# Optimization experiments

Measured on AMD Instinct MI355X. Metric: run time of the kernel, lower is better.

The kernel has to match this reference:

```python
import jax, jax.numpy as jnp
import numpy as np

B, MENU, N, M = 4096, 256, 8, 16


def setup_inputs() -> dict:
    key = jax.random.key(0)
    k1, k2, k3, k4 = jax.random.split(key, 4)
    input_bids = jax.random.uniform(k1, (B, N, M), dtype=jnp.float32)
    allocs = jax.random.uniform(k2, (B, MENU, N, M), dtype=jnp.float32)
    # bidder weights must be strictly positive (divided by in payments)
    w = jax.random.uniform(k3, (B, N), dtype=jnp.float32, minval=0.5, maxval=1.5)
    b = jax.random.normal(k4, (B, MENU), dtype=jnp.float32)
    softmax_temp = jnp.asarray(100.0, dtype=jnp.float32)
    return {"input_bids": input_bids, "allocs": allocs, "w": w, "b": b,
            "softmax_temp": softmax_temp}


def reference(input_bids, allocs, w, b, softmax_temp):
    Bsz, n, m = input_bids.shape
    # append the "null" menu entry (zero allocation, zero boost)
    allocs = jnp.concatenate([allocs, jnp.zeros((Bsz, 1, n, m), allocs.dtype)], axis=1)  # B,S,n,m
    b = jnp.concatenate([b, jnp.zeros((Bsz, 1), b.dtype)], axis=1)                        # B,S

    # utility of each agent under each menu entry
    util = jnp.einsum('bsnm,bnm->bsn', allocs, input_bids)        # B,S,n
    per_agent_welfare = w[:, None, :] * util                      # B,S,n
    total_welfare = per_agent_welfare.sum(-1)                     # B,S

    alloc_choice = jax.nn.softmax((total_welfare + b) * softmax_temp, axis=-1)  # B,S
    item_allocation = jnp.einsum('bs,bsnm->bnm', alloc_choice, allocs)          # B,n,m
    chosen_welfare = jnp.einsum('bsn,bs->bn', per_agent_welfare, alloc_choice)  # B,n

    # leave-one-out (VCG-style) payments, vectorized over the removed agent i
    mask = 1.0 - jnp.eye(n, dtype=per_agent_welfare.dtype)        # n,n; row i zeros agent i
    removed_welfare = per_agent_welfare[None] * mask[:, None, None, :]  # i,B,S,n
    total_removed = removed_welfare.sum(-1)                       # i,B,S
    removed_choice = jax.nn.softmax((total_removed + b[None]) * softmax_temp, axis=-1)  # i,B,S

    removed_chosen_sum = jnp.einsum('ibsn,ibs->ib', removed_welfare, removed_choice)  # i,B
    masked_chosen_sum = jnp.einsum('bn,in->ib', chosen_welfare, mask)                 # i,B
    removed_b = jnp.einsum('ibs,bs->ib', removed_choice, b)                           # i,B
    alloc_b = jnp.einsum('bs,bs->b', alloc_choice, b)                                 # B

    payments = (removed_chosen_sum + removed_b - masked_chosen_sum - alloc_b[None]) / w.T  # n,B
    return alloc_choice, item_allocation, payments, allocs
```

## Files before the change

kernel.cpp:

```cpp
#include <hip/hip_runtime.h>

#define NAGENTS 8
#define NM 128
#define MENU 256
#define SFULL 257

#define BAR() asm volatile("s_waitcnt lgkmcnt(0)\n\ts_barrier" ::: "memory")

__device__ __forceinline__ float wredmax(float v) {
#pragma unroll
    for (int o = 32; o; o >>= 1) v = fmaxf(v, __shfl_xor(v, o));
    return v;
}
__device__ __forceinline__ float wredsum(float v) {
#pragma unroll
    for (int o = 32; o; o >>= 1) v += __shfl_xor(v, o);
    return v;
}

__global__ __launch_bounds__(1024, 4) void cama_kernel(
    const float* __restrict__ bids,
    const float* __restrict__ allocs,
    const float* __restrict__ wvec,
    const float* __restrict__ bvec,
    const float* __restrict__ tempp,
    float* __restrict__ out, int Bsz, int iters)
{
    __shared__ float lds_pwT[NAGENTS * MENU];
    __shared__ float lds_tot[MENU];
    __shared__ float lds_bb[2][MENU];
    __shared__ __align__(16) float lds_bids[2][NM];
    __shared__ float lds_w[2][NAGENTS];
    __shared__ float lds_ch[SFULL];
    __shared__ __align__(16) float lds_scr[16 * NM];
    __shared__ float lds_rcs[NAGENTS], lds_rb[NAGENTS], lds_cw[NAGENTS];
    __shared__ float lds_ab;

    const int u = threadIdx.x;
    const int lane = u & 63;
    const int wave = u >> 6;
    const int n  = (u >> 2) & 7;
    const int mq = u & 3;
    const int su = u >> 5;

    float* out_choice = out;
    float* out_item   = out + (size_t)Bsz * SFULL;
    float* out_pay    = out_item + (size_t)Bsz * NM;
    float* out_all    = out_pay + (size_t)NAGENTS * Bsz;
    float4* out_all4  = (float4*)out_all;
    const float4* all4 = (const float4*)allocs;

    const float temp = tempp[0];
    size_t a = (size_t)blockIdx.x * iters;

    float4 Pf[8];

    {
        float rbb = 0.f, rbid = 0.f, rw = 0.f;
        if (u < MENU)    rbb  = bvec[a * MENU + u];
        if (u < NM)      rbid = bids[a * NM + u];
        if (u < NAGENTS) rw   = wvec[a * NAGENTS + u];
#pragma unroll
        for (int k = 0; k < 8; ++k)
            Pf[k] = all4[a * 8192 + (k << 10) + u];
        if (u < MENU)    lds_bb[0][u]   = rbb;
        if (u < NM)      lds_bids[0][u] = rbid;
        if (u < NAGENTS) lds_w[0][u]    = rw;
    }
    BAR();

    for (int it = 0; it < iters; ++it) {
        const int p = it & 1;
        const size_t an = (it + 1 < iters) ? a + 1 : a;

        const float4 q4 = ((const float4*)&lds_bids[p][0])[u & 31];
        const float w_n = lds_w[p][n];

        float4 Sf[8];
#pragma unroll
        for (int k = 0; k < 8; ++k) {
            Sf[k] = Pf[k];
            Pf[k] = all4[an * 8192 + (k << 10) + u];
            out_all4[a * 8224 + (k << 10) + u] = Sf[k];
            const int s = (k << 5) + su;
            float util = Sf[k].x*q4.x + Sf[k].y*q4.y + Sf[k].z*q4.z + Sf[k].w*q4.w;
            util += __shfl_xor(util, 1);
            util += __shfl_xor(util, 2);
            float pwv = w_n * util;
            if (mq == 0) lds_pwT[(n << 8) + (s ^ (n << 2))] = pwv;
            float t = pwv;
            t += __shfl_xor(t, 4);
            t += __shfl_xor(t, 8);
            t += __shfl_xor(t, 16);
            if ((lane & 31) == 0) lds_tot[s] = t;
        }
        if (u < 32)
            out_all4[a * 8224 + 8192 + u] = make_float4(0.f, 0.f, 0.f, 0.f);

        float rbb2 = 0.f, rbid2 = 0.f, rw2 = 0.f;
        if (u < MENU)    rbb2  = bvec[an * MENU + u];
        if (u < NM)      rbid2 = bids[an * NM + u];
        if (u < NAGENTS) rw2   = wvec[an * NAGENTS + u];
        BAR();

        if (wave == 0) {
            float xs[4], bl[4], es[4];
            float mx = -1e30f;
#pragma unroll
            for (int c = 0; c < 4; ++c) {
                int v = (c << 6) | lane;
                bl[c] = lds_bb[p][v];
                float x = (lds_tot[v] + bl[c]) * temp;
                xs[c] = x; mx = fmaxf(mx, x);
            }
            mx = fmaxf(wredmax(mx), 0.f);
            float se = 0.f, sab = 0.f;
#pragma unroll
            for (int c = 0; c < 4; ++c) { es[c] = __expf(xs[c] - mx); se += es[c]; sab += es[c] * bl[c]; }
            float en = __expf(-mx);
            se = wredsum(se) + en;
            sab = wredsum(sab);
            float inv = 1.f / se;
#pragma unroll
            for (int c = 0; c < 4; ++c) {
                int v = (c << 6) | lane;
                float chv = es[c] * inv;
                lds_ch[v] = chv;
                out_choice[a * SFULL + v] = chv;
            }
            if (lane == 0) {
                float chn = en * inv;
                lds_ch[MENU] = chn;
                out_choice[a * SFULL + MENU] = chn;
                lds_ab = sab * inv;
            }
        } else if (wave <= 8) {
            const int i = wave - 1;
            float xs[4], trs[4], bl[4];
            float mx = -1e30f;
#pragma unroll
            for (int c = 0; c < 4; ++c) {
                int v = (c << 6) | lane;
                bl[c] = lds_bb[p][v];
                float tr = lds_tot[v] - lds_pwT[(i << 8) + (v ^ (i << 2))];
                trs[c] = tr;
                float x = (tr + bl[c]) * temp;
                xs[c] = x; mx = fmaxf(mx, x);
            }
            mx = fmaxf(wredmax(mx), 0.f);
            float se = 0.f, s1 = 0.f, s2 = 0.f;
#pragma unroll
            for (int c = 0; c < 4; ++c) {
                float e = __expf(xs[c] - mx);
                se += e; s1 += e * trs[c]; s2 += e * bl[c];
            }
            se = wredsum(se) + __expf(-mx);
            s1 = wredsum(s1);
            s2 = wredsum(s2);
            if (lane == 0) { lds_rcs[i] = s1 / se; lds_rb[i] = s2 / se; }
        }
        BAR();

        if (wave < 8) {
            const int i = wave;
            float cwv = 0.f;
#pragma unroll
            for (int c = 0; c < 4; ++c) {
                int v = (c << 6) | lane;
                cwv += lds_ch[v] * lds_pwT[(i << 8) + (v ^ (i << 2))];
            }
            cwv = wredsum(cwv);
            if (lane == 0) lds_cw[i] = cwv;
        }
        {
            float ax = 0.f, ay = 0.f, az = 0.f, aw = 0.f;
#pragma unroll
            for (int k = 0; k < 8; ++k) {
                float chv = lds_ch[(k << 5) + su];
                ax += Sf[k].x * chv; ay += Sf[k].y * chv;
                az += Sf[k].z * chv; aw += Sf[k].w * chv;
            }
            ax += __shfl_xor(ax, 32);
            ay += __shfl_xor(ay, 32);
            az += __shfl_xor(az, 32);
            aw += __shfl_xor(aw, 32);
            if (lane < 32)
                ((float4*)lds_scr)[(wave << 5) + lane] = make_float4(ax, ay, az, aw);
        }
        if (u < MENU)    lds_bb[p ^ 1][u]   = rbb2;
        if (u < NM)      lds_bids[p ^ 1][u] = rbid2;
        if (u < NAGENTS) lds_w[p ^ 1][u]    = rw2;
        BAR();

        if (u < NM) {
            float s = 0.f;
#pragma unroll
            for (int w = 0; w < 16; ++w) s += lds_scr[(w << 7) + u];
            out_item[a * NM + u] = s;
        }
        if (u < NAGENTS) {
            float ctot = 0.f;
#pragma unroll
            for (int k = 0; k < NAGENTS; ++k) ctot += lds_cw[k];
            float pay = (lds_rcs[u] + lds_rb[u] - (ctot - lds_cw[u]) - lds_ab)
                        / lds_w[p][u];
            out_pay[(size_t)u * Bsz + a] = pay;
        }
        a = a + 1;
    }
}

extern "C" void kernel_launch(void* const* d_in, const int* in_sizes, int n_in,
                              void* d_out, int out_size, void* d_ws, size_t ws_size,
                              hipStream_t stream) {
    const float* bids   = (const float*)d_in[0];
    const float* allocs = (const float*)d_in[1];
    const float* wvec   = (const float*)d_in[2];
    const float* bvec   = (const float*)d_in[3];
    const float* tempp  = (const float*)d_in[4];
    float* out = (float*)d_out;
    const int Bsz = in_sizes[0] / NM;
    const int nblocks = 256;
    const int iters = Bsz / nblocks;
    cama_kernel<<<nblocks, 1024, 0, stream>>>(bids, allocs, wvec, bvec, tempp,
                                              out, Bsz, iters);
}
```

Measured before the change: 259.6 us.

## Use one 256-thread block per batch row with online-softmax item allocation

Replaces the persistent 256-block, 1024-thread kernel that software-pipelined allocs loads across iterations with one 256-thread block per batch element. The item allocation is now accumulated during the streaming pass with an online (running max / rescaled) softmax, then merged across halves and waves. This removes the register-held allocs tile and one barrier phase. In exchange it drops the explicit cross-iteration prefetch and relies on many resident blocks to hide memory latency, and it adds extra exp work per element.

New measurement: 235.3 us. -9.4%, faster.

```diff
diff --git a/kernel.cpp b/kernel.cpp
--- a/kernel.cpp
+++ b/kernel.cpp
@@ -18,195 +18,202 @@
     return v;
 }
 
-__global__ __launch_bounds__(1024, 4) void cama_kernel(
+__global__ __launch_bounds__(256, 8) void cama_kernel(
     const float* __restrict__ bids,
     const float* __restrict__ allocs,
     const float* __restrict__ wvec,
     const float* __restrict__ bvec,
     const float* __restrict__ tempp,
-    float* __restrict__ out, int Bsz, int iters)
+    float* __restrict__ out, int Bsz)
 {
     __shared__ float lds_pwT[NAGENTS * MENU];
     __shared__ float lds_tot[MENU];
-    __shared__ float lds_bb[2][MENU];
-    __shared__ __align__(16) float lds_bids[2][NM];
-    __shared__ float lds_w[2][NAGENTS];
+    __shared__ float lds_bb[MENU];
     __shared__ float lds_ch[SFULL];
-    __shared__ __align__(16) float lds_scr[16 * NM];
+    __shared__ __align__(16) float4 lds_accs[4][32];
+    __shared__ __align__(8)  float2 lds_mz[4][32];
     __shared__ float lds_rcs[NAGENTS], lds_rb[NAGENTS], lds_cw[NAGENTS];
     __shared__ float lds_ab;
 
     const int u = threadIdx.x;
     const int lane = u & 63;
     const int wave = u >> 6;
-    const int n  = (u >> 2) & 7;
-    const int mq = u & 3;
+    const int c = u & 31;
+    const int n = c >> 2;
     const int su = u >> 5;
+    const size_t bb_ = (size_t)blockIdx.x;
 
     float* out_choice = out;
     float* out_item   = out + (size_t)Bsz * SFULL;
     float* out_pay    = out_item + (size_t)Bsz * NM;
     float* out_all    = out_pay + (size_t)NAGENTS * Bsz;
-    float4* out_all4  = (float4*)out_all;
-    const float4* all4 = (const float4*)allocs;
+    float4* out_all4  = (float4*)out_all + bb_ * 8224;
+    const float4* src4 = (const float4*)allocs + bb_ * 8192;
 
     const float temp = tempp[0];
-    size_t a = (size_t)blockIdx.x * iters;
-
-    float4 Pf[8];
+    lds_bb[u] = bvec[bb_ * MENU + u];
+    const float4 q4 = ((const float4*)(bids + bb_ * NM))[c];
+    const float w_n = wvec[bb_ * NAGENTS + n];
+    BAR();
+
+    float m_r = -1e30f, Z_r = 0.f;
+    float4 acc = make_float4(0.f, 0.f, 0.f, 0.f);
+#pragma unroll 4
+    for (int k = 0; k < 32; ++k) {
+        const int idx = (k << 8) + u;
+        float4 a4 = src4[idx];
+        out_all4[idx] = a4;
+        const int s = (k << 3) + su;
+        float util = a4.x*q4.x + a4.y*q4.y + a4.z*q4.z + a4.w*q4.w;
+        util += __shfl_xor(util, 1);
+        util += __shfl_xor(util, 2);
+        float pwv = w_n * util;
+        if ((u & 3) == 0) lds_pwT[(n << 8) + (s ^ (n << 2))] = pwv;
+        float t = pwv;
+        t += __shfl_xor(t, 4);
+        t += __shfl_xor(t, 8);
+        t += __shfl_xor(t, 16);
+        if (c == 0) lds_tot[s] = t;
+        float x = (t + lds_bb[s]) * temp;
+        float mn = fmaxf(m_r, x);
+        float sc = __expf(m_r - mn);
+        float p  = __expf(x - mn);
+        Z_r = Z_r * sc + p;
+        acc.x = acc.x * sc + p * a4.x;
+        acc.y = acc.y * sc + p * a4.y;
+        acc.z = acc.z * sc + p * a4.z;
+        acc.w = acc.w * sc + p * a4.w;
+        m_r = mn;
+    }
+    if (u < 32)
+        out_all4[8192 + u] = make_float4(0.f, 0.f, 0.f, 0.f);
 
     {
-        float rbb = 0.f, rbid = 0.f, rw = 0.f;
-        if (u < MENU)    rbb  = bvec[a * MENU + u];
-        if (u < NM)      rbid = bids[a * NM + u];
-        if (u < NAGENTS) rw   = wvec[a * NAGENTS + u];
-#pragma unroll
-        for (int k = 0; k < 8; ++k)
-            Pf[k] = all4[a * 8192 + (k << 10) + u];
-        if (u < MENU)    lds_bb[0][u]   = rbb;
-        if (u < NM)      lds_bids[0][u] = rbid;
-        if (u < NAGENTS) lds_w[0][u]    = rw;
-    }
-    BAR();
-
-    for (int it = 0; it < iters; ++it) {
-        const int p = it & 1;
-        const size_t an = (it + 1 < iters) ? a + 1 : a;
-
-        const float4 q4 = ((const float4*)&lds_bids[p][0])[u & 31];
-        const float w_n = lds_w[p][n];
-
-        float4 Sf[8];
-#pragma unroll
-        for (int k = 0; k < 8; ++k) {
-            Sf[k] = Pf[k];
-            Pf[k] = all4[an * 8192 + (k << 10) + u];
-            out_all4[a * 8224 + (k << 10) + u] = Sf[k];
-            const int s = (k << 5) + su;
-            float util = Sf[k].x*q4.x + Sf[k].y*q4.y + Sf[k].z*q4.z + Sf[k].w*q4.w;
-            util += __shfl_xor(util, 1);
-            util += __shfl_xor(util, 2);
-            float pwv = w_n * util;
-            if (mq == 0) lds_pwT[(n << 8) + (s ^ (n << 2))] = pwv;
-            float t = pwv;
-            t += __shfl_xor(t, 4);
-            t += __shfl_xor(t, 8);
-            t += __shfl_xor(t, 16);
-            if ((lane & 31) == 0) lds_tot[s] = t;
-        }
-        if (u < 32)
-            out_all4[a * 8224 + 8192 + u] = make_float4(0.f, 0.f, 0.f, 0.f);
-
-        float rbb2 = 0.f, rbid2 = 0.f, rw2 = 0.f;
-        if (u < MENU)    rbb2  = bvec[an * MENU + u];
-        if (u < NM)      rbid2 = bids[an * NM + u];
-        if (u < NAGENTS) rw2   = wvec[an * NAGENTS + u];
-        BAR();
-
-        if (wave == 0) {
+        float mo = __shfl_xor(m_r, 32);
+        float Zo = __shfl_xor(Z_r, 32);
+        float ax = __shfl_xor(acc.x, 32), ay = __shfl_xor(acc.y, 32);
+        float az = __shfl_xor(acc.z, 32), aw = __shfl_xor(acc.w, 32);
+        float mn = fmaxf(m_r, mo);
+        float s0 = __expf(m_r - mn), s1 = __expf(mo - mn);
+        Z_r = Z_r * s0 + Zo * s1;
+        acc.x = acc.x * s0 + ax * s1;
+        acc.y = acc.y * s0 + ay * s1;
+        acc.z = acc.z * s0 + az * s1;
+        acc.w = acc.w * s0 + aw * s1;
+        if (lane < 32) {
+            lds_accs[wave][c] = acc;
+            lds_mz[wave][c] = make_float2(mn, Z_r);
+        }
+    }
+    BAR();
+
+    for (int t = wave; t < 9; t += 4) {
+        if (t == 0) {
             float xs[4], bl[4], es[4];
             float mx = -1e30f;
 #pragma unroll
-            for (int c = 0; c < 4; ++c) {
-                int v = (c << 6) | lane;
-                bl[c] = lds_bb[p][v];
-                float x = (lds_tot[v] + bl[c]) * temp;
-                xs[c] = x; mx = fmaxf(mx, x);
+            for (int c4 = 0; c4 < 4; ++c4) {
+                int v = (c4 << 6) | lane;
+                bl[c4] = lds_bb[v];
+                float x = (lds_tot[v] + bl[c4]) * temp;
+                xs[c4] = x; mx = fmaxf(mx, x);
             }
             mx = fmaxf(wredmax(mx), 0.f);
             float se = 0.f, sab = 0.f;
 #pragma unroll
-            for (int c = 0; c < 4; ++c) { es[c] = __expf(xs[c] - mx); se += es[c]; sab += es[c] * bl[c]; }
+            for (int c4 = 0; c4 < 4; ++c4) {
+                es[c4] = __expf(xs[c4] - mx);
+                se += es[c4]; sab += es[c4] * bl[c4];
+            }
             float en = __expf(-mx);
             se = wredsum(se) + en;
             sab = wredsum(sab);
             float inv = 1.f / se;
 #pragma unroll
-            for (int c = 0; c < 4; ++c) {
-                int v = (c << 6) | lane;
-                float chv = es[c] * inv;
+            for (int c4 = 0; c4 < 4; ++c4) {
+                int v = (c4 << 6) | lane;
+                float chv = es[c4] * inv;
                 lds_ch[v] = chv;
-                out_choice[a * SFULL + v] = chv;
+                out_choice[bb_ * SFULL + v] = chv;
             }
             if (lane == 0) {
                 float chn = en * inv;
                 lds_ch[MENU] = chn;
-                out_choice[a * SFULL + MENU] = chn;
+                out_choice[bb_ * SFULL + MENU] = chn;
                 lds_ab = sab * inv;
             }
-        } else if (wave <= 8) {
-            const int i = wave - 1;
+        } else {
+            const int i = t - 1;
             float xs[4], trs[4], bl[4];
             float mx = -1e30f;
 #pragma unroll
-            for (int c = 0; c < 4; ++c) {
-                int v = (c << 6) | lane;
-                bl[c] = lds_bb[p][v];
+            for (int c4 = 0; c4 < 4; ++c4) {
+                int v = (c4 << 6) | lane;
+                bl[c4] = lds_bb[v];
                 float tr = lds_tot[v] - lds_pwT[(i << 8) + (v ^ (i << 2))];
-                trs[c] = tr;
-                float x = (tr + bl[c]) * temp;
-                xs[c] = x; mx = fmaxf(mx, x);
+                trs[c4] = tr;
+                float x = (tr + bl[c4]) * temp;
+                xs[c4] = x; mx = fmaxf(mx, x);
             }
             mx = fmaxf(wredmax(mx), 0.f);
             float se = 0.f, s1 = 0.f, s2 = 0.f;
 #pragma unroll
-            for (int c = 0; c < 4; ++c) {
-                float e = __expf(xs[c] - mx);
-                se += e; s1 += e * trs[c]; s2 += e * bl[c];
+            for (int c4 = 0; c4 < 4; ++c4) {
+                float e = __expf(xs[c4] - mx);
+                se += e; s1 += e * trs[c4]; s2 += e * bl[c4];
             }
             se = wredsum(se) + __expf(-mx);
             s1 = wredsum(s1);
             s2 = wredsum(s2);
             if (lane == 0) { lds_rcs[i] = s1 / se; lds_rb[i] = s2 / se; }
         }
-        BAR();
-
-        if (wave < 8) {
-            const int i = wave;
-            float cwv = 0.f;
-#pragma unroll
-            for (int c = 0; c < 4; ++c) {
-                int v = (c << 6) | lane;
-                cwv += lds_ch[v] * lds_pwT[(i << 8) + (v ^ (i << 2))];
-            }
-            cwv = wredsum(cwv);
-            if (lane == 0) lds_cw[i] = cwv;
-        }
-        {
-            float ax = 0.f, ay = 0.f, az = 0.f, aw = 0.f;
-#pragma unroll
-            for (int k = 0; k < 8; ++k) {
-                float chv = lds_ch[(k << 5) + su];
-                ax += Sf[k].x * chv; ay += Sf[k].y * chv;
-                az += Sf[k].z * chv; aw += Sf[k].w * chv;
-            }
-            ax += __shfl_xor(ax, 32);
-            ay += __shfl_xor(ay, 32);
-            az += __shfl_xor(az, 32);
-            aw += __shfl_xor(aw, 32);
-            if (lane < 32)
-                ((float4*)lds_scr)[(wave << 5) + lane] = make_float4(ax, ay, az, aw);
-        }
-        if (u < MENU)    lds_bb[p ^ 1][u]   = rbb2;
-        if (u < NM)      lds_bids[p ^ 1][u] = rbid2;
-        if (u < NAGENTS) lds_w[p ^ 1][u]    = rw2;
-        BAR();
-
-        if (u < NM) {
-            float s = 0.f;
-#pragma unroll
-            for (int w = 0; w < 16; ++w) s += lds_scr[(w << 7) + u];
-            out_item[a * NM + u] = s;
-        }
-        if (u < NAGENTS) {
-            float ctot = 0.f;
-#pragma unroll
-            for (int k = 0; k < NAGENTS; ++k) ctot += lds_cw[k];
-            float pay = (lds_rcs[u] + lds_rb[u] - (ctot - lds_cw[u]) - lds_ab)
-                        / lds_w[p][u];
-            out_pay[(size_t)u * Bsz + a] = pay;
-        }
-        a = a + 1;
+    }
+    BAR();
+
+    for (int i = wave; i < NAGENTS; i += 4) {
+        float cwv = 0.f;
+#pragma unroll
+        for (int c4 = 0; c4 < 4; ++c4) {
+            int v = (c4 << 6) | lane;
+            cwv += lds_ch[v] * lds_pwT[(i << 8) + (v ^ (i << 2))];
+        }
+        cwv = wredsum(cwv);
+        if (lane == 0) lds_cw[i] = cwv;
+    }
+    if (u < 32) {
+        float4 A = lds_accs[0][u];
+        float2 mz = lds_mz[0][u];
+        float M = mz.x, Z = mz.y;
+#pragma unroll
+        for (int j = 1; j < 4; ++j) {
+            float4 Aj = lds_accs[j][u];
+            float2 mzj = lds_mz[j][u];
+            float mn = fmaxf(M, mzj.x);
+            float s0 = __expf(M - mn), s1 = __expf(mzj.x - mn);
+            Z = Z * s0 + mzj.y * s1;
+            A.x = A.x * s0 + Aj.x * s1;
+            A.y = A.y * s0 + Aj.y * s1;
+            A.z = A.z * s0 + Aj.z * s1;
+            A.w = A.w * s0 + Aj.w * s1;
+            M = mn;
+        }
+        float mn = fmaxf(M, 0.f);
+        float s0 = __expf(M - mn);
+        Z = Z * s0 + __expf(-mn);
+        float inv = 1.f / Z;
+        s0 *= inv;
+        ((float4*)(out_item + bb_ * NM))[u] =
+            make_float4(A.x * s0, A.y * s0, A.z * s0, A.w * s0);
+    }
+    BAR();
+
+    if (u < NAGENTS) {
+        float ctot = 0.f;
+#pragma unroll
+        for (int k = 0; k < NAGENTS; ++k) ctot += lds_cw[k];
+        float pay = (lds_rcs[u] + lds_rb[u] - (ctot - lds_cw[u]) - lds_ab)
+                    / wvec[bb_ * NAGENTS + u];
+        out_pay[(size_t)u * Bsz + bb_] = pay;
     }
 }
 
@@ -220,8 +227,6 @@
     const float* tempp  = (const float*)d_in[4];
     float* out = (float*)d_out;
     const int Bsz = in_sizes[0] / NM;
-    const int nblocks = 256;
-    const int iters = Bsz / nblocks;
-    cama_kernel<<<nblocks, 1024, 0, stream>>>(bids, allocs, wvec, bvec, tempp,
-                                              out, Bsz, iters);
-}
+    cama_kernel<<<Bsz, 256, 0, stream>>>(bids, allocs, wvec, bvec, tempp,
+                                         out, Bsz);
+}
```
